# Kernel optimization log

Measured on AMD Instinct MI355X. Metric: run time of the kernel, lower is better.

The kernel has to match this reference:

```python
import jax, jax.numpy as jnp
import numpy as np

B, P, G = 32, 19248, 32
NUM_CLASSES = 41          # 40 foreground + background (index 0)
POS_TH, NEG_TH = 0.5, 0.4
NEGPOS_RATIO = 3
BBOX_ALPHA = 1.5
CONF_ALPHA = 6.5
VAR_C, VAR_S = 0.1, 0.2   # SSD encoding variances


def point_form(b):
    # (cx,cy,w,h) -> (x1,y1,x2,y2)
    return jnp.concatenate([b[:, :2] - b[:, 2:] / 2, b[:, :2] + b[:, 2:] / 2], axis=-1)


def jaccard(a, b):
    # a: [G,4], b: [P,4] point-form -> IoU [G,P]
    lt = jnp.maximum(a[:, None, :2], b[None, :, :2])
    rb = jnp.minimum(a[:, None, 2:], b[None, :, 2:])
    wh = jnp.clip(rb - lt, 0.0)
    inter = wh[..., 0] * wh[..., 1]
    area_a = ((a[:, 2] - a[:, 0]) * (a[:, 3] - a[:, 1]))[:, None]
    area_b = ((b[:, 2] - b[:, 0]) * (b[:, 3] - b[:, 1]))[None, :]
    return inter / (area_a + area_b - inter)


def encode(matched, priors):
    # matched: [P,4] point-form gt, priors: [P,4] center-size
    g_cxcy = ((matched[:, :2] + matched[:, 2:]) / 2 - priors[:, :2]) / (VAR_C * priors[:, 2:])
    g_wh = jnp.log(jnp.clip((matched[:, 2:] - matched[:, :2]) / priors[:, 2:], 1e-8)) / VAR_S
    return jnp.concatenate([g_cxcy, g_wh], axis=-1)


def match_one(gt_box, gt_label, priors_pf, priors):
    ov = jaccard(gt_box, priors_pf)                     # [G,P]
    best_truth_ov = ov.max(axis=0)                      # [P]
    best_truth_idx = ov.argmax(axis=0)                  # [P]
    best_prior_idx = ov.argmax(axis=1)                  # [G]
    # force each gt to keep its best prior
    best_truth_ov = best_truth_ov.at[best_prior_idx].set(2.0)
    best_truth_idx = best_truth_idx.at[best_prior_idx].set(jnp.arange(G))
    matched = gt_box[best_truth_idx]                    # [P,4]
    conf = gt_label[best_truth_idx] + 1                 # background = 0
    conf = jnp.where(best_truth_ov < POS_TH, -1, conf)  # neutral band
    conf = jnp.where(best_truth_ov < NEG_TH, 0, conf)   # negatives
    return encode(matched, priors), conf


def smooth_l1(x, t):
    d = jnp.abs(x - t)
    return jnp.where(d < 1.0, 0.5 * d * d, d - 0.5)


def setup_inputs() -> dict:
    key = jax.random.key(0)
    ks = jax.random.split(key, 7)
    loc_data = jax.random.normal(ks[0], (B, P, 4), dtype=jnp.float32) * 0.5
    conf_data = jax.random.normal(ks[1], (B, P, NUM_CLASSES), dtype=jnp.float32)
    cxcy = jax.random.uniform(ks[2], (P, 2), minval=0.02, maxval=0.98)
    wh = jax.random.uniform(ks[3], (P, 2), minval=0.05, maxval=0.4)
    priors = jnp.concatenate([cxcy, wh], axis=-1)
    gc = jax.random.uniform(ks[4], (B, G, 2), minval=0.2, maxval=0.8)
    gwh = jax.random.uniform(ks[5], (B, G, 2), minval=0.05, maxval=0.4)
    gt_bboxes = jnp.clip(jnp.concatenate([gc - gwh / 2, gc + gwh / 2], axis=-1), 0.0, 1.0)
    gt_labels = jax.random.randint(ks[6], (B, G), 0, 40)
    return {"loc_data": loc_data, "conf_data": conf_data, "priors": priors,
            "gt_bboxes": gt_bboxes, "gt_labels": gt_labels}


def reference(loc_data, conf_data, priors, gt_bboxes, gt_labels):
    priors_pf = point_form(priors)
    loc_t, conf_t = jax.vmap(match_one, in_axes=(0, 0, None, None))(
        gt_bboxes, gt_labels, priors_pf, priors)        # [B,P,4], [B,P]
    loc_t = jax.lax.stop_gradient(loc_t)                # targets are constants
    pos = conf_t > 0                                    # [B,P]
    num_pos = jnp.maximum(pos.sum(), 1).astype(loc_data.dtype)

    # localization loss: mean over positives of per-prior smooth-L1 (summed over 4)
    box_l = smooth_l1(loc_data, loc_t).sum(-1)          # [B,P]
    loss_B = (box_l * pos).sum() / num_pos * BBOX_ALPHA

    # hard negative mining on background confidence loss
    lse = jax.nn.logsumexp(conf_data, axis=-1)          # [B,P]
    tgt = jnp.clip(conf_t, 0)
    picked = jnp.take_along_axis(conf_data, tgt[..., None], axis=-1).squeeze(-1)
    loss_c = lse - picked                               # CE per prior
    mined = jnp.where(pos | (conf_t < 0), 0.0, loss_c)  # zero out pos & neutral
    order = jnp.argsort(-mined, axis=1)
    rank = jnp.argsort(order, axis=1)                   # rank of each prior by loss
    num_neg = jnp.clip(NEGPOS_RATIO * pos.sum(axis=1), 0, P - 1)  # [B]
    neg = (rank < num_neg[:, None]) & (conf_t == 0)

    keep = (pos | neg).astype(loc_data.dtype)
    loss_C = (loss_c * keep).sum() / num_pos * CONF_ALPHA
    return loss_B + loss_C
```

## Files before the change

kernel.cpp:

```cpp
#include <hip/hip_runtime.h>

static constexpr int B = 32;
static constexpr int P = 19248;
static constexpr int G = 32;
static constexpr int C = 41;
static constexpr float POS_TH = 0.5f;
static constexpr float NEG_TH = 0.4f;

static constexpr int TM = 128;
static constexpr int PBM = (P + TM - 1) / TM;
static constexpr int NPART = 8;
static constexpr int PPART = P / NPART;
static constexpr int P4 = P / 4;

__device__ __forceinline__ float sl1(float d) {
    d = fabsf(d);
    return d < 1.0f ? 0.5f * d * d : d - 0.5f;
}

__device__ __forceinline__ unsigned long long umax64(unsigned long long a,
                                                     unsigned long long b) {
    return a > b ? a : b;
}

__global__ __launch_bounds__(1024) void k_match(
    const float* __restrict__ priors, const float* __restrict__ gt,
    unsigned long long* __restrict__ bp_part, int* __restrict__ done) {
    int part = blockIdx.x, b = blockIdx.y;
    if (part == 0 && b == 0 && threadIdx.x == 0) *done = 0;
    int lane = threadIdx.x & 63, wid = threadIdx.x >> 6;
    int pbase = part * PPART;

    int g0 = wid, g1 = wid + 16;
    float4 gb0 = reinterpret_cast<const float4*>(gt)[b * G + g0];
    float4 gb1 = reinterpret_cast<const float4*>(gt)[b * G + g1];
    float ga0 = (gb0.z - gb0.x) * (gb0.w - gb0.y);
    float ga1 = (gb1.z - gb1.x) * (gb1.w - gb1.y);

    float best0 = -1.0f, best1 = -1.0f;
    int bi0 = 0, bi1 = 0;
    for (int i = lane; i < PPART; i += 64) {
        int p = pbase + i;
        float4 pr = reinterpret_cast<const float4*>(priors)[p];
        float px1 = pr.x - pr.z * 0.5f, py1 = pr.y - pr.w * 0.5f;
        float px2 = pr.x + pr.z * 0.5f, py2 = pr.y + pr.w * 0.5f;
        float parea = (px2 - px1) * (py2 - py1);
        {
            float lx = fmaxf(gb0.x, px1), ly = fmaxf(gb0.y, py1);
            float rx = fminf(gb0.z, px2), ry = fminf(gb0.w, py2);
            float w = fmaxf(rx - lx, 0.0f), h = fmaxf(ry - ly, 0.0f);
            float inter = w * h;
            float iou = __fdividef(inter, ga0 + parea - inter);
            if (iou > best0) { best0 = iou; bi0 = p; }
        }
        {
            float lx = fmaxf(gb1.x, px1), ly = fmaxf(gb1.y, py1);
            float rx = fminf(gb1.z, px2), ry = fminf(gb1.w, py2);
            float w = fmaxf(rx - lx, 0.0f), h = fmaxf(ry - ly, 0.0f);
            float inter = w * h;
            float iou = __fdividef(inter, ga1 + parea - inter);
            if (iou > best1) { best1 = iou; bi1 = p; }
        }
    }
    unsigned long long pk0 =
        ((unsigned long long)__float_as_uint(best0) << 32)
        | (unsigned)(0xFFFFFFFFu - (unsigned)bi0);
    unsigned long long pk1 =
        ((unsigned long long)__float_as_uint(best1) << 32)
        | (unsigned)(0xFFFFFFFFu - (unsigned)bi1);
#pragma unroll
    for (int d = 32; d; d >>= 1) {
        unsigned long long o0 = __shfl_xor(pk0, d);
        unsigned long long o1 = __shfl_xor(pk1, d);
        if (o0 > pk0) pk0 = o0;
        if (o1 > pk1) pk1 = o1;
    }
    if (lane == 0) {
        bp_part[(part * B + b) * G + g0] = pk0;
        bp_part[(part * B + b) * G + g1] = pk1;
    }
}

__global__ __launch_bounds__(TM) void k_main(
    const float* __restrict__ loc_data, const float* __restrict__ conf_data,
    const float* __restrict__ priors, const float* __restrict__ gt,
    const int* __restrict__ labels,
    const unsigned long long* __restrict__ bp_part,
    float* __restrict__ mined, float4* __restrict__ partial) {
    int b = blockIdx.y;
    int p0 = blockIdx.x * TM;
    int tid = threadIdx.x;
    int p = p0 + tid;
    int lane = tid & 63, wid = tid >> 6;
    __shared__ float sconf[TM * C];
    __shared__ int sforce[G];
    __shared__ float4 sg[G];
    __shared__ float sarea[G];

    if (tid < G) {
        unsigned long long mx = 0ull;
#pragma unroll
        for (int q = 0; q < NPART; ++q) {
            unsigned long long v = bp_part[(q * B + b) * G + tid];
            mx = umax64(mx, v);
        }
        sforce[tid] = (int)(0xFFFFFFFFu - (unsigned)mx);
        float4 g4 = reinterpret_cast<const float4*>(gt)[b * G + tid];
        sg[tid] = g4;
        sarea[tid] = (g4.z - g4.x) * (g4.w - g4.y);
    }
    __syncthreads();

    int valid = min(TM, P - p0);
    size_t gbase = ((size_t)b * P + p0) * C;
    int tot4 = (valid * C) >> 2;
    const float4* g4p = reinterpret_cast<const float4*>(conf_data + gbase);
    float4* s4 = reinterpret_cast<float4*>(sconf);
#if defined(__has_builtin) && __has_builtin(__builtin_amdgcn_global_load_lds)
    typedef const __attribute__((address_space(1))) char* gas1_t;
    typedef __attribute__((address_space(3))) char* las3_t;
#define GL(j) { int i = tid + (j) * TM; if (i < tot4) \
    __builtin_amdgcn_global_load_lds((gas1_t)(g4p + i), (las3_t)(s4 + i), 16, 0, 0); }
    GL(0) GL(1) GL(2) GL(3) GL(4) GL(5) GL(6) GL(7) GL(8) GL(9) GL(10)
#undef GL
#define STAGE_WAIT asm volatile("s_waitcnt vmcnt(0)" ::: "memory")
#else
    float4 r0, r1, r2, r3, r4, r5, r6, r7, r8, r9, r10;
#define LD(j, rj) { int i = tid + (j) * TM; if (i < tot4) rj = g4p[i]; }
    LD(0, r0) LD(1, r1) LD(2, r2) LD(3, r3) LD(4, r4) LD(5, r5)
    LD(6, r6) LD(7, r7) LD(8, r8) LD(9, r9) LD(10, r10)
#undef LD
#define STAGE_WAIT do { \
    int i; \
    i = tid + 0*TM;  if (i < tot4) s4[i] = r0; \
    i = tid + 1*TM;  if (i < tot4) s4[i] = r1; \
    i = tid + 2*TM;  if (i < tot4) s4[i] = r2; \
    i = tid + 3*TM;  if (i < tot4) s4[i] = r3; \
    i = tid + 4*TM;  if (i < tot4) s4[i] = r4; \
    i = tid + 5*TM;  if (i < tot4) s4[i] = r5; \
    i = tid + 6*TM;  if (i < tot4) s4[i] = r6; \
    i = tid + 7*TM;  if (i < tot4) s4[i] = r7; \
    i = tid + 8*TM;  if (i < tot4) s4[i] = r8; \
    i = tid + 9*TM;  if (i < tot4) s4[i] = r9; \
    i = tid + 10*TM; if (i < tot4) s4[i] = r10; \
} while (0)
#endif

    float my_box = 0.0f, my_posc = 0.0f; int my_pos = 0;
    bool pos = false, neutral = false;
    int cls = 0;
    if (p < P) {
        float4 pr = reinterpret_cast<const float4*>(priors)[p];
        float px1 = pr.x - pr.z * 0.5f, py1 = pr.y - pr.w * 0.5f;
        float px2 = pr.x + pr.z * 0.5f, py2 = pr.y + pr.w * 0.5f;
        float parea = (px2 - px1) * (py2 - py1);
        float ov = -1.0f; int bidx = 0;
#pragma unroll
        for (int g = 0; g < G; ++g) {
            float4 gb = sg[g];
            float lx = fmaxf(gb.x, px1), ly = fmaxf(gb.y, py1);
            float rx = fminf(gb.z, px2), ry = fminf(gb.w, py2);
            float w = fmaxf(rx - lx, 0.0f), h = fmaxf(ry - ly, 0.0f);
            float inter = w * h;
            float iou = __fdividef(inter, sarea[g] + parea - inter);
            if (iou > ov) { ov = iou; bidx = g; }
        }
        int fidx = -1;
#pragma unroll
        for (int g = 0; g < G; ++g)
            if (p == sforce[g]) fidx = g;
        int gidx = 0;
        if (fidx >= 0)            { pos = true; gidx = fidx; }
        else if (ov >= POS_TH)    { pos = true; gidx = bidx; }
        else if (ov >= NEG_TH)    { neutral = true; }
        if (pos) {
            cls = labels[b * G + gidx] + 1;
            float4 gb = sg[gidx];
            float mcx = (gb.x + gb.z) * 0.5f, mcy = (gb.y + gb.w) * 0.5f;
            float tx = (mcx - pr.x) / (0.1f * pr.z);
            float ty = (mcy - pr.y) / (0.1f * pr.w);
            float tw = __logf(fmaxf((gb.z - gb.x) / pr.z, 1e-8f)) / 0.2f;
            float th = __logf(fmaxf((gb.w - gb.y) / pr.w, 1e-8f)) / 0.2f;
            float4 ld = reinterpret_cast<const float4*>(loc_data)[b * P + p];
            my_box = sl1(ld.x - tx) + sl1(ld.y - ty) + sl1(ld.z - tw) + sl1(ld.w - th);
        }
        my_pos = pos ? 1 : 0;
    }

    STAGE_WAIT;
#undef STAGE_WAIT
    __syncthreads();

    if (p < P) {
        const float* cv = &sconf[tid * C];
        float mx = cv[0];
#pragma unroll
        for (int c = 1; c < C; ++c) mx = fmaxf(mx, cv[c]);
        float se = 0.0f;
#pragma unroll
        for (int c = 0; c < C; ++c) se += __expf(cv[c] - mx);
        float lse = mx + __logf(se);
        float lc = lse - cv[cls];
        mined[(size_t)b * P + p] = (pos || neutral) ? 0.0f : lc;
        my_posc = pos ? lc : 0.0f;
    }

#pragma unroll
    for (int d = 32; d; d >>= 1) {
        my_box  += __shfl_xor(my_box, d);
        my_posc += __shfl_xor(my_posc, d);
        my_pos  += __shfl_xor(my_pos, d);
    }
    __shared__ float rb[2], rc[2]; __shared__ int rp[2];
    if (lane == 0) { rb[wid] = my_box; rc[wid] = my_posc; rp[wid] = my_pos; }
    __syncthreads();
    if (tid == 0) {
        partial[b * PBM + blockIdx.x] =
            make_float4(rb[0] + rb[1], rc[0] + rc[1], (float)(rp[0] + rp[1]), 0.0f);
    }
}

__global__ __launch_bounds__(1024) void k_topk(
    const float* __restrict__ mined, const float4* __restrict__ partial,
    float* __restrict__ neg_b, int* __restrict__ done,
    float* __restrict__ out) {
    int b = blockIdx.x;
    const float4* mb4 = reinterpret_cast<const float4*>(mined + (size_t)b * P);
    int tid = threadIdx.x;
    int lane = tid & 63, wid = tid >> 6;

    int cnt = 0;
    if (tid < PBM) cnt = (int)partial[b * PBM + tid].z;
#pragma unroll
    for (int d = 32; d; d >>= 1) cnt += __shfl_xor(cnt, d);
    __shared__ int ired[16];
    if (lane == 0) ired[wid] = cnt;
    __syncthreads();
    int np = 0;
#pragma unroll
    for (int w2 = 0; w2 < 16; ++w2) np += ired[w2];
    int k = 3 * np; if (k > P - 1) k = P - 1;

    float negval = 0.0f;
    if (k > 0) {
        __shared__ unsigned hist[2048];
        __shared__ unsigned sel[3];
        __shared__ unsigned wtot[16];
        __shared__ unsigned zcs;
        if (tid == 0) { sel[0] = 0u; sel[1] = (unsigned)k; sel[2] = 0u; }
        const int shifts[3] = {21, 10, 0};
        const int widths[3] = {11, 11, 10};
#pragma unroll
        for (int level = 0; level < 3; ++level) {
            int shift = shifts[level];
            unsigned bmask = (1u << widths[level]) - 1u;
            hist[tid] = 0u; hist[tid + 1024] = 0u;
            __syncthreads();
            unsigned pref = sel[0];
            unsigned pmask = level ? (0xFFFFFFFFu << (shift + widths[level])) : 0u;
            unsigned zc = 0;
            for (int i = tid; i < P4; i += 1024) {
                float4 v4 = mb4[i];
                unsigned v;
                v = __float_as_uint(v4.x);
                if (v) { if ((v & pmask) == pref) atomicAdd(&hist[(v >> shift) & bmask], 1u); }
                else ++zc;
                v = __float_as_uint(v4.y);
                if (v) { if ((v & pmask) == pref) atomicAdd(&hist[(v >> shift) & bmask], 1u); }
                else ++zc;
                v = __float_as_uint(v4.z);
                if (v) { if ((v & pmask) == pref) atomicAdd(&hist[(v >> shift) & bmask], 1u); }
                else ++zc;
                v = __float_as_uint(v4.w);
                if (v) { if ((v & pmask) == pref) atomicAdd(&hist[(v >> shift) & bmask], 1u); }
                else ++zc;
            }
            if (level == 0) {
#pragma unroll
                for (int d = 32; d; d >>= 1) zc += __shfl_xor(zc, d);
                if (lane == 0) wtot[wid] = zc;
                __syncthreads();
                if (tid == 0) {
                    unsigned t = 0;
#pragma unroll
                    for (int w2 = 0; w2 < 16; ++w2) t += wtot[w2];
                    zcs = t;
                }
            }
            __syncthreads();
            if (tid == 0 && pref == 0u) hist[0] += zcs;
            __syncthreads();
            unsigned h0 = hist[2 * tid], h1 = hist[2 * tid + 1];
            unsigned x = h0 + h1;
#pragma unroll
            for (int d = 1; d < 64; d <<= 1) {
                unsigned t = __shfl_down(x, d);
                if (lane + d < 64) x += t;
            }
            if (lane == 0) wtot[wid] = x;
            __syncthreads();
            unsigned above = 0;
            for (int w2 = wid + 1; w2 < 16; ++w2) above += wtot[w2];
            unsigned sp = x + above;
            unsigned s2 = sp - h0 - h1;
            unsigned s1 = s2 + h1;
            unsigned want = sel[1];
            __syncthreads();
            if (s1 >= want && s2 < want) {
                sel[0] = pref | (((2u * (unsigned)tid + 1u) & bmask) << shift);
                sel[1] = want - s2;
                sel[2] += s2;
            } else if (sp >= want && s1 < want) {
                sel[0] = pref | (((2u * (unsigned)tid) & bmask) << shift);
                sel[1] = want - s1;
                sel[2] += s1;
            }
            __syncthreads();
        }
        unsigned vk = sel[0];
        unsigned cnt_gt = sel[2];
        float vkf = __uint_as_float(vk);
        float ssum = 0.0f;
        for (int i = tid; i < P4; i += 1024) {
            float4 v4 = mb4[i];
            if (__float_as_uint(v4.x) > vk) ssum += v4.x;
            if (__float_as_uint(v4.y) > vk) ssum += v4.y;
            if (__float_as_uint(v4.z) > vk) ssum += v4.z;
            if (__float_as_uint(v4.w) > vk) ssum += v4.w;
        }
#pragma unroll
        for (int d = 32; d; d >>= 1) ssum += __shfl_xor(ssum, d);
        __shared__ float rs[16];
        if (lane == 0) rs[wid] = ssum;
        __syncthreads();
        if (tid == 0) {
            float tot = 0.0f;
#pragma unroll
            for (int w2 = 0; w2 < 16; ++w2) tot += rs[w2];
            negval = tot + (float)(k - (int)cnt_gt) * vkf;
        }
    }

    __shared__ bool islast;
    if (tid == 0) {
        neg_b[b] = negval;
        __threadfence();
        int old = atomicAdd(done, 1);
        islast = (old == B - 1);
    }
    __syncthreads();
    if (!islast) return;
    __threadfence();

    float sbx = 0.0f, sc = 0.0f, sp2 = 0.0f, sn = 0.0f;
    for (int i = tid; i < B * PBM; i += 1024) {
        float4 v = partial[i];
        sbx += v.x; sc += v.y; sp2 += v.z;
    }
    if (tid < B) sn = neg_b[tid];
#pragma unroll
    for (int d = 32; d; d >>= 1) {
        sbx += __shfl_xor(sbx, d);
        sc  += __shfl_xor(sc, d);
        sp2 += __shfl_xor(sp2, d);
        sn  += __shfl_xor(sn, d);
    }
    __shared__ float fr[16][4];
    if (lane == 0) { fr[wid][0] = sbx; fr[wid][1] = sc; fr[wid][2] = sp2; fr[wid][3] = sn; }
    __syncthreads();
    if (tid == 0) {
        float tb = 0, tc = 0, tp = 0, tn = 0;
#pragma unroll
        for (int w2 = 0; w2 < 16; ++w2) {
            tb += fr[w2][0]; tc += fr[w2][1]; tp += fr[w2][2]; tn += fr[w2][3];
        }
        float npos = fmaxf(tp, 1.0f);
        out[0] = tb / npos * 1.5f + (tc + tn) / npos * 6.5f;
    }
}

extern "C" void kernel_launch(void* const* d_in, const int* in_sizes, int n_in,
                              void* d_out, int out_size, void* d_ws, size_t ws_size,
                              hipStream_t stream) {
    const float* loc    = (const float*)d_in[0];
    const float* conf   = (const float*)d_in[1];
    const float* priors = (const float*)d_in[2];
    const float* gt     = (const float*)d_in[3];
    const int*   labels = (const int*)d_in[4];
    float* out = (float*)d_out;

    char* w = (char*)d_ws;
    float4* partial = (float4*)w;                      w += sizeof(float4) * B * PBM;
    float* mined  = (float*)w;                         w += sizeof(float) * B * P;
    unsigned long long* bp_part = (unsigned long long*)w;
    w += sizeof(unsigned long long) * NPART * B * G;
    float* negb   = (float*)w;                         w += sizeof(float) * B;
    int*   done   = (int*)w;                           w += sizeof(int);

    k_match<<<dim3(NPART, B), 1024, 0, stream>>>(priors, gt, bp_part, done);
    k_main<<<dim3(PBM, B), TM, 0, stream>>>(loc, conf, priors, gt, labels,
                                            bp_part, mined, partial);
    k_topk<<<B, 1024, 0, stream>>>(mined, partial, negb, done, out);
}
```

Before: 77.56 us.

## Fuse match and main kernels; apply forced-prior matches as corrections in top-k

Merges the per-gt best-prior search into the main per-prior kernel as extra interleaved blocks, so main blocks no longer wait on a prior kernel for forced-match indices. The forced-match override is deferred to the top-k kernel, which recomputes each forced prior's loss contributions and applies delta corrections to the positive count, box loss and class loss, and zeroes its mined value. This removes one launch and the dependency between the match pass and the main pass. The cost is a serial correction step in top-k and extra indexing logic. There is a possible read ordering issue because mined is overwritten while it is also read through a restrict-qualified alias.

```diff
diff --git a/kernel.cpp b/kernel.cpp
--- a/kernel.cpp
+++ b/kernel.cpp
@@ -13,6 +13,10 @@
 static constexpr int PPART = P / NPART;
 static constexpr int P4 = P / 4;
 
+static constexpr int NB_MATCH = NPART * 8 * B;
+static constexpr int NB_MAIN  = B * PBM;
+static constexpr int NB_TOT   = NB_MATCH + NB_MAIN;
+
 __device__ __forceinline__ float sl1(float d) {
     d = fabsf(d);
     return d < 1.0f ? 0.5f * d * d : d - 0.5f;
@@ -23,88 +27,89 @@
     return a > b ? a : b;
 }
 
-__global__ __launch_bounds__(1024) void k_match(
-    const float* __restrict__ priors, const float* __restrict__ gt,
-    unsigned long long* __restrict__ bp_part, int* __restrict__ done) {
-    int part = blockIdx.x, b = blockIdx.y;
-    if (part == 0 && b == 0 && threadIdx.x == 0) *done = 0;
-    int lane = threadIdx.x & 63, wid = threadIdx.x >> 6;
-    int pbase = part * PPART;
-
-    int g0 = wid, g1 = wid + 16;
-    float4 gb0 = reinterpret_cast<const float4*>(gt)[b * G + g0];
-    float4 gb1 = reinterpret_cast<const float4*>(gt)[b * G + g1];
-    float ga0 = (gb0.z - gb0.x) * (gb0.w - gb0.y);
-    float ga1 = (gb1.z - gb1.x) * (gb1.w - gb1.y);
-
-    float best0 = -1.0f, best1 = -1.0f;
-    int bi0 = 0, bi1 = 0;
-    for (int i = lane; i < PPART; i += 64) {
-        int p = pbase + i;
-        float4 pr = reinterpret_cast<const float4*>(priors)[p];
-        float px1 = pr.x - pr.z * 0.5f, py1 = pr.y - pr.w * 0.5f;
-        float px2 = pr.x + pr.z * 0.5f, py2 = pr.y + pr.w * 0.5f;
-        float parea = (px2 - px1) * (py2 - py1);
-        {
-            float lx = fmaxf(gb0.x, px1), ly = fmaxf(gb0.y, py1);
-            float rx = fminf(gb0.z, px2), ry = fminf(gb0.w, py2);
-            float w = fmaxf(rx - lx, 0.0f), h = fmaxf(ry - ly, 0.0f);
-            float inter = w * h;
-            float iou = __fdividef(inter, ga0 + parea - inter);
-            if (iou > best0) { best0 = iou; bi0 = p; }
-        }
-        {
-            float lx = fmaxf(gb1.x, px1), ly = fmaxf(gb1.y, py1);
-            float rx = fminf(gb1.z, px2), ry = fminf(gb1.w, py2);
-            float w = fmaxf(rx - lx, 0.0f), h = fmaxf(ry - ly, 0.0f);
-            float inter = w * h;
-            float iou = __fdividef(inter, ga1 + parea - inter);
-            if (iou > best1) { best1 = iou; bi1 = p; }
-        }
-    }
-    unsigned long long pk0 =
-        ((unsigned long long)__float_as_uint(best0) << 32)
-        | (unsigned)(0xFFFFFFFFu - (unsigned)bi0);
-    unsigned long long pk1 =
-        ((unsigned long long)__float_as_uint(best1) << 32)
-        | (unsigned)(0xFFFFFFFFu - (unsigned)bi1);
-#pragma unroll
-    for (int d = 32; d; d >>= 1) {
-        unsigned long long o0 = __shfl_xor(pk0, d);
-        unsigned long long o1 = __shfl_xor(pk1, d);
-        if (o0 > pk0) pk0 = o0;
-        if (o1 > pk1) pk1 = o1;
-    }
-    if (lane == 0) {
-        bp_part[(part * B + b) * G + g0] = pk0;
-        bp_part[(part * B + b) * G + g1] = pk1;
-    }
-}
-
-__global__ __launch_bounds__(TM) void k_main(
+__global__ __launch_bounds__(TM) void k_fused(
     const float* __restrict__ loc_data, const float* __restrict__ conf_data,
     const float* __restrict__ priors, const float* __restrict__ gt,
     const int* __restrict__ labels,
-    const unsigned long long* __restrict__ bp_part,
-    float* __restrict__ mined, float4* __restrict__ partial) {
-    int b = blockIdx.y;
-    int p0 = blockIdx.x * TM;
+    unsigned long long* __restrict__ bp_part,
+    float* __restrict__ mined, float4* __restrict__ partial,
+    int* __restrict__ done) {
+    int bid = blockIdx.x;
     int tid = threadIdx.x;
-    int p = p0 + tid;
     int lane = tid & 63, wid = tid >> 6;
+
+    int f0 = (bid * NB_MATCH) / NB_TOT;
+    int f1 = ((bid + 1) * NB_MATCH) / NB_TOT;
+    bool is_match = (f1 != f0);
+
+    if (is_match) {
+        int mid = f0;
+        if (mid == 0 && tid == 0) *done = 0;
+        int part = mid & 7;
+        int gq   = (mid >> 3) & 7;
+        int b    = mid >> 6;
+        int pbase = part * PPART;
+        int g0 = gq * 4 + 2 * wid;
+        int g1 = g0 + 1;
+        float4 gb0 = reinterpret_cast<const float4*>(gt)[b * G + g0];
+        float4 gb1 = reinterpret_cast<const float4*>(gt)[b * G + g1];
+        float ga0 = (gb0.z - gb0.x) * (gb0.w - gb0.y);
+        float ga1 = (gb1.z - gb1.x) * (gb1.w - gb1.y);
+        float best0 = -1.0f, best1 = -1.0f;
+        int bi0 = 0, bi1 = 0;
+        for (int i = lane; i < PPART; i += 64) {
+            int p = pbase + i;
+            float4 pr = reinterpret_cast<const float4*>(priors)[p];
+            float px1 = pr.x - pr.z * 0.5f, py1 = pr.y - pr.w * 0.5f;
+            float px2 = pr.x + pr.z * 0.5f, py2 = pr.y + pr.w * 0.5f;
+            float parea = (px2 - px1) * (py2 - py1);
+            {
+                float lx = fmaxf(gb0.x, px1), ly = fmaxf(gb0.y, py1);
+                float rx = fminf(gb0.z, px2), ry = fminf(gb0.w, py2);
+                float w = fmaxf(rx - lx, 0.0f), h = fmaxf(ry - ly, 0.0f);
+                float inter = w * h;
+                float iou = __fdividef(inter, ga0 + parea - inter);
+                if (iou > best0) { best0 = iou; bi0 = p; }
+            }
+            {
+                float lx = fmaxf(gb1.x, px1), ly = fmaxf(gb1.y, py1);
+                float rx = fminf(gb1.z, px2), ry = fminf(gb1.w, py2);
+                float w = fmaxf(rx - lx, 0.0f), h = fmaxf(ry - ly, 0.0f);
+                float inter = w * h;
+                float iou = __fdividef(inter, ga1 + parea - inter);
+                if (iou > best1) { best1 = iou; bi1 = p; }
+            }
+        }
+        unsigned long long pk0 =
+            ((unsigned long long)__float_as_uint(best0) << 32)
+            | (unsigned)(0xFFFFFFFFu - (unsigned)bi0);
+        unsigned long long pk1 =
+            ((unsigned long long)__float_as_uint(best1) << 32)
+            | (unsigned)(0xFFFFFFFFu - (unsigned)bi1);
+#pragma unroll
+        for (int d = 32; d; d >>= 1) {
+            unsigned long long o0 = __shfl_xor(pk0, d);
+            unsigned long long o1 = __shfl_xor(pk1, d);
+            if (o0 > pk0) pk0 = o0;
+            if (o1 > pk1) pk1 = o1;
+        }
+        if (lane == 0) {
+            bp_part[(part * B + b) * G + g0] = pk0;
+            bp_part[(part * B + b) * G + g1] = pk1;
+        }
+        return;
+    }
+
+    int mainid = bid - f0;
+    int b  = mainid / PBM;
+    int bx = mainid - b * PBM;
+    int p0 = bx * TM;
+    int p  = p0 + tid;
     __shared__ float sconf[TM * C];
-    __shared__ int sforce[G];
     __shared__ float4 sg[G];
     __shared__ float sarea[G];
 
     if (tid < G) {
-        unsigned long long mx = 0ull;
-#pragma unroll
-        for (int q = 0; q < NPART; ++q) {
-            unsigned long long v = bp_part[(q * B + b) * G + tid];
-            mx = umax64(mx, v);
-        }
-        sforce[tid] = (int)(0xFFFFFFFFu - (unsigned)mx);
         float4 g4 = reinterpret_cast<const float4*>(gt)[b * G + tid];
         sg[tid] = g4;
         sarea[tid] = (g4.z - g4.x) * (g4.w - g4.y);
@@ -165,14 +170,9 @@
             float iou = __fdividef(inter, sarea[g] + parea - inter);
             if (iou > ov) { ov = iou; bidx = g; }
         }
-        int fidx = -1;
-#pragma unroll
-        for (int g = 0; g < G; ++g)
-            if (p == sforce[g]) fidx = g;
         int gidx = 0;
-        if (fidx >= 0)            { pos = true; gidx = fidx; }
-        else if (ov >= POS_TH)    { pos = true; gidx = bidx; }
-        else if (ov >= NEG_TH)    { neutral = true; }
+        if (ov >= POS_TH)       { pos = true; gidx = bidx; }
+        else if (ov >= NEG_TH)  { neutral = true; }
         if (pos) {
             cls = labels[b * G + gidx] + 1;
             float4 gb = sg[gidx];
@@ -215,20 +215,112 @@
     if (lane == 0) { rb[wid] = my_box; rc[wid] = my_posc; rp[wid] = my_pos; }
     __syncthreads();
     if (tid == 0) {
-        partial[b * PBM + blockIdx.x] =
+        partial[b * PBM + bx] =
             make_float4(rb[0] + rb[1], rc[0] + rc[1], (float)(rp[0] + rp[1]), 0.0f);
     }
 }
 
 __global__ __launch_bounds__(1024) void k_topk(
     const float* __restrict__ mined, const float4* __restrict__ partial,
-    float* __restrict__ neg_b, int* __restrict__ done,
+    const unsigned long long* __restrict__ bp_part,
+    const float* __restrict__ loc_data, const float* __restrict__ conf_data,
+    const float* __restrict__ priors, const float* __restrict__ gt,
+    const int* __restrict__ labels,
+    float* __restrict__ mined_mut,
+    float4* __restrict__ corr, int* __restrict__ done,
     float* __restrict__ out) {
     int b = blockIdx.x;
     const float4* mb4 = reinterpret_cast<const float4*>(mined + (size_t)b * P);
     int tid = threadIdx.x;
     int lane = tid & 63, wid = tid >> 6;
 
+    __shared__ float4 sgt[G];
+    __shared__ float sga[G];
+    __shared__ int sfp[G];
+    __shared__ float scorr[3];
+
+    if (tid < G) {
+        unsigned long long mx = 0ull;
+#pragma unroll
+        for (int q = 0; q < NPART; ++q)
+            mx = umax64(mx, bp_part[(q * B + b) * G + tid]);
+        sfp[tid] = (int)(0xFFFFFFFFu - (unsigned)mx);
+        float4 g4 = reinterpret_cast<const float4*>(gt)[b * G + tid];
+        sgt[tid] = g4;
+        sga[tid] = (g4.z - g4.x) * (g4.w - g4.y);
+    }
+    __syncthreads();
+
+    float dnp_f = 0.0f, dbox_f = 0.0f, dposc_f = 0.0f;
+    if (tid < G) {
+        int g = tid;
+        int pfx = sfp[g];
+        bool alive = true;
+        for (int g2 = g + 1; g2 < G; ++g2)
+            if (sfp[g2] == pfx) { alive = false; break; }
+        if (alive) {
+            int p = pfx;
+            float4 pr = reinterpret_cast<const float4*>(priors)[p];
+            float px1 = pr.x - pr.z * 0.5f, py1 = pr.y - pr.w * 0.5f;
+            float px2 = pr.x + pr.z * 0.5f, py2 = pr.y + pr.w * 0.5f;
+            float parea = (px2 - px1) * (py2 - py1);
+            float ov = -1.0f; int bidx = 0;
+#pragma unroll
+            for (int g2 = 0; g2 < G; ++g2) {
+                float4 gb = sgt[g2];
+                float lx = fmaxf(gb.x, px1), ly = fmaxf(gb.y, py1);
+                float rx = fminf(gb.z, px2), ry = fminf(gb.w, py2);
+                float w = fmaxf(rx - lx, 0.0f), h = fmaxf(ry - ly, 0.0f);
+                float inter = w * h;
+                float iou = __fdividef(inter, sga[g2] + parea - inter);
+                if (iou > ov) { ov = iou; bidx = g2; }
+            }
+            bool pos_u = (ov >= POS_TH);
+            const float* cv = conf_data + ((size_t)b * P + p) * C;
+            float mx = cv[0];
+#pragma unroll
+            for (int c = 1; c < C; ++c) mx = fmaxf(mx, cv[c]);
+            float se = 0.0f;
+#pragma unroll
+            for (int c = 0; c < C; ++c) se += __expf(cv[c] - mx);
+            float lse = mx + __logf(se);
+            float4 ld = reinterpret_cast<const float4*>(loc_data)[b * P + p];
+            auto boxl = [&](const float4& gb) {
+                float mcx = (gb.x + gb.z) * 0.5f, mcy = (gb.y + gb.w) * 0.5f;
+                float tx = (mcx - pr.x) / (0.1f * pr.z);
+                float ty = (mcy - pr.y) / (0.1f * pr.w);
+                float tw = __logf(fmaxf((gb.z - gb.x) / pr.z, 1e-8f)) / 0.2f;
+                float th = __logf(fmaxf((gb.w - gb.y) / pr.w, 1e-8f)) / 0.2f;
+                return sl1(ld.x - tx) + sl1(ld.y - ty) + sl1(ld.z - tw) + sl1(ld.w - th);
+            };
+            int cls_f = labels[b * G + g] + 1;
+            float lc_f = lse - cv[cls_f];
+            float box_f = boxl(sgt[g]);
+            float box_u = 0.0f, lc_u = 0.0f;
+            if (pos_u) {
+                int cls_u = labels[b * G + bidx] + 1;
+                lc_u = lse - cv[cls_u];
+                box_u = boxl(sgt[bidx]);
+            }
+            dnp_f   = pos_u ? 0.0f : 1.0f;
+            dbox_f  = box_f - box_u;
+            dposc_f = lc_f - lc_u;
+            mined_mut[(size_t)b * P + p] = 0.0f;
+        }
+    }
+    if (wid == 0) {
+#pragma unroll
+        for (int d = 32; d; d >>= 1) {
+            dnp_f   += __shfl_xor(dnp_f, d);
+            dbox_f  += __shfl_xor(dbox_f, d);
+            dposc_f += __shfl_xor(dposc_f, d);
+        }
+        if (lane == 0) { scorr[0] = dbox_f; scorr[1] = dposc_f; scorr[2] = dnp_f; }
+    }
+    __threadfence_block();
+    __syncthreads();
+    float dboxT = scorr[0], dposcT = scorr[1], dnpT = scorr[2];
+
     int cnt = 0;
     if (tid < PBM) cnt = (int)partial[b * PBM + tid].z;
 #pragma unroll
@@ -236,7 +328,7 @@
     __shared__ int ired[16];
     if (lane == 0) ired[wid] = cnt;
     __syncthreads();
-    int np = 0;
+    int np = (int)dnpT;
 #pragma unroll
     for (int w2 = 0; w2 < 16; ++w2) np += ired[w2];
     int k = 3 * np; if (k > P - 1) k = P - 1;
@@ -343,7 +435,7 @@
 
     __shared__ bool islast;
     if (tid == 0) {
-        neg_b[b] = negval;
+        corr[b] = make_float4(negval, dboxT, dposcT, dnpT);
         __threadfence();
         int old = atomicAdd(done, 1);
         islast = (old == B - 1);
@@ -357,7 +449,10 @@
         float4 v = partial[i];
         sbx += v.x; sc += v.y; sp2 += v.z;
     }
-    if (tid < B) sn = neg_b[tid];
+    if (tid < B) {
+        float4 cr = corr[tid];
+        sn += cr.x; sbx += cr.y; sc += cr.z; sp2 += cr.w;
+    }
 #pragma unroll
     for (int d = 32; d; d >>= 1) {
         sbx += __shfl_xor(sbx, d);
@@ -394,11 +489,12 @@
     float* mined  = (float*)w;                         w += sizeof(float) * B * P;
     unsigned long long* bp_part = (unsigned long long*)w;
     w += sizeof(unsigned long long) * NPART * B * G;
-    float* negb   = (float*)w;                         w += sizeof(float) * B;
+    float4* corr  = (float4*)w;                        w += sizeof(float4) * B;
     int*   done   = (int*)w;                           w += sizeof(int);
 
-    k_match<<<dim3(NPART, B), 1024, 0, stream>>>(priors, gt, bp_part, done);
-    k_main<<<dim3(PBM, B), TM, 0, stream>>>(loc, conf, priors, gt, labels,
-                                            bp_part, mined, partial);
-    k_topk<<<B, 1024, 0, stream>>>(mined, partial, negb, done, out);
+    k_fused<<<NB_TOT, TM, 0, stream>>>(loc, conf, priors, gt, labels,
+                                       bp_part, mined, partial, done);
+    k_topk<<<B, 1024, 0, stream>>>(mined, partial, bp_part,
+                                   loc, conf, priors, gt, labels,
+                                   mined, corr, done, out);
 }
```

Measured after the change: 95.30 us. +22.9%, slower.
